# Kernel optimization log

Hardware: AMD Instinct MI355X
Metric: run time of the kernel (lower is better)

## Reference

```python
import jax, jax.numpy as jnp
import numpy as np

DIM = 128
HEADS = 4
DH = 32
SCALE = DH ** -0.5


def _ln(x, g, b):
    m = x.mean(-1, keepdims=True)
    v = x.var(-1, keepdims=True)
    return (x - m) / jnp.sqrt(v + 1e-5) * g + b


def setup_inputs() -> dict:
    key = jax.random.key(0)
    ks = jax.random.split(key, 16)
    B, N, H, W, HK, WK = 2, 6, 48, 48, 24, 24
    d, hd = DIM, HEADS * DH
    p = lambda k, s: (jax.random.normal(k, s, jnp.float32) * 0.02)
    return {
        "q": jax.random.normal(ks[0], (B, N, d, H, W), jnp.float32),
        "k": jax.random.normal(ks[1], (B, N, d, HK, WK), jnp.float32),
        "v": jax.random.normal(ks[2], (B, N, d, HK, WK), jnp.float32),
        "skip": jax.random.normal(ks[3], (B, d, H, W), jnp.float32),
        "lnq_g": jnp.ones(d), "lnq_b": jnp.zeros(d),
        "Wq": p(ks[4], (d, hd)), "bq": jnp.zeros(hd),
        "lnk_g": jnp.ones(d), "lnk_b": jnp.zeros(d),
        "Wk": p(ks[5], (d, hd)), "bk": jnp.zeros(hd),
        "lnv_g": jnp.ones(d), "lnv_b": jnp.zeros(d),
        "Wv": p(ks[6], (d, hd)), "bv": jnp.zeros(hd),
        "Wp": p(ks[7], (hd, d)), "bp": jnp.zeros(d),
        "pre_g": jnp.ones(d), "pre_b": jnp.zeros(d),
        "W1": p(ks[8], (d, 2 * d)), "b1": jnp.zeros(2 * d),
        "W2": p(ks[9], (2 * d, d)), "b2": jnp.zeros(d),
        "post_g": jnp.ones(d), "post_b": jnp.zeros(d),
    }


def reference(q, k, v, skip, lnq_g, lnq_b, Wq, bq, lnk_g, lnk_b, Wk, bk,
              lnv_g, lnv_b, Wv, bv, Wp, bp, pre_g, pre_b, W1, b1, W2, b2,
              post_g, post_b):
    B, N, d, H, W = q.shape
    _, _, _, HK, WK = k.shape
    Q, K = H * W, HK * WK
    # b n d H W -> b n (H W) d
    qx = q.transpose(0, 1, 3, 4, 2).reshape(B, N, Q, d)
    kx = k.transpose(0, 1, 3, 4, 2).reshape(B, N, K, d)
    vx = v.transpose(0, 1, 3, 4, 2).reshape(B, N * K, d)
    # norm + linear projections
    qp = _ln(qx, lnq_g, lnq_b) @ Wq + bq  # (B,N,Q,HEADS*DH)
    kp = _ln(kx, lnk_g, lnk_b) @ Wk + bk
    vp = _ln(vx, lnv_g, lnv_b) @ Wv + bv  # (B,N*K,HEADS*DH)
    # split heads: b ... (m d) -> (b m) ... d
    qp = qp.reshape(B, N, Q, HEADS, DH).transpose(0, 3, 1, 2, 4).reshape(B * HEADS, N, Q, DH)
    kp = kp.reshape(B, N, K, HEADS, DH).transpose(0, 3, 1, 2, 4).reshape(B * HEADS, N, K, DH)
    vp = vp.reshape(B, N * K, HEADS, DH).transpose(0, 2, 1, 3).reshape(B * HEADS, N * K, DH)
    # per-view scores, then softmax jointly over (n K)
    scores = SCALE * jnp.einsum('bnqd,bnkd->bnqk', qp, kp)
    scores = scores.transpose(0, 2, 1, 3).reshape(B * HEADS, Q, N * K)
    a = jax.nn.softmax(scores, axis=-1)
    out = jnp.einsum('bqk,bkd->bqd', a, vp)  # (B*HEADS, Q, DH)
    # merge heads: (b m) Q d -> b Q (m d)
    z = out.reshape(B, HEADS, Q, DH).transpose(0, 2, 1, 3).reshape(B, Q, HEADS * DH)
    z = z @ Wp + bp
    z = z + skip.transpose(0, 2, 3, 1).reshape(B, Q, d)
    z = _ln(z, pre_g, pre_b)
    z = z + (jax.nn.gelu(z @ W1 + b1, approximate=False) @ W2 + b2)
    z = _ln(z, post_g, post_b)
    return z.reshape(B, H, W, d).transpose(0, 3, 1, 2)
```

## Files before the change

### kernel.cpp

```cpp
#include <hip/hip_runtime.h>
#include <cmath>

#define B_    2
#define N_    6
#define D_    128
#define Q_    2304
#define K_    576
#define NK_   3456
#define HEADS_ 4
#define DH_   32
#define SCALE_ 0.17677669529663687f

typedef __attribute__((ext_vector_type(8))) short bf16x8;
typedef __attribute__((ext_vector_type(4))) float f32x4;

static __device__ __forceinline__ unsigned short f2bf(float f) {
  union { float f; unsigned u; } x; x.f = f;
  unsigned u = x.u + 0x7fffu + ((x.u >> 16) & 1u);
  return (unsigned short)(u >> 16);
}
static __device__ __forceinline__ unsigned pkbf(float a, float b) {
  return (unsigned)f2bf(a) | ((unsigned)f2bf(b) << 16);
}

__global__ __launch_bounds__(256) void k_prep_wt(
    const float* __restrict__ Wq, const float* __restrict__ Wk,
    const float* __restrict__ Wv, const float* __restrict__ Wp,
    const float* __restrict__ W1, const float* __restrict__ W2,
    unsigned short* __restrict__ WTq, unsigned short* __restrict__ WTk,
    unsigned short* __restrict__ WTv, unsigned short* __restrict__ WTp,
    unsigned short* __restrict__ WT1, unsigned short* __restrict__ WT2)
{
  __shared__ float tile[32][33];
  const int wb = blockIdx.x, t = threadIdx.x;
  const float* src; unsigned short* dst; int Kd, J, tl;
  if      (wb < 16) { src = Wq; dst = WTq; Kd = 128; J = 128; tl = wb; }
  else if (wb < 32) { src = Wk; dst = WTk; Kd = 128; J = 128; tl = wb - 16; }
  else if (wb < 48) { src = Wv; dst = WTv; Kd = 128; J = 128; tl = wb - 32; }
  else if (wb < 64) { src = Wp; dst = WTp; Kd = 128; J = 128; tl = wb - 48; }
  else if (wb < 96) { src = W1; dst = WT1; Kd = 128; J = 256; tl = wb - 64; }
  else              { src = W2; dst = WT2; Kd = 256; J = 128; tl = wb - 96; }
  const int njt = J >> 5;
  const int tj = tl % njt, tk = tl / njt;
#pragma unroll
  for (int i = 0; i < 4; ++i) {
    int idx = t + 256 * i;
    int r = idx >> 5, c = idx & 31;
    tile[r][c] = src[(size_t)(tk * 32 + r) * J + tj * 32 + c];
  }
  __syncthreads();
#pragma unroll
  for (int i = 0; i < 2; ++i) {
    int idx = t + 256 * i;
    int rr = idx >> 4, c2 = (idx & 15) << 1;
    *(unsigned*)&dst[(size_t)(tj * 32 + rr) * Kd + tk * 32 + c2] =
        pkbf(tile[c2][rr], tile[c2 + 1][rr]);
  }
}

__global__ __launch_bounds__(256) void k_ln_proj_all(
    const float* __restrict__ qin, const float* __restrict__ kin,
    const float* __restrict__ vin,
    const float* __restrict__ lnq_g, const float* __restrict__ lnq_b,
    const float* __restrict__ lnk_g, const float* __restrict__ lnk_b,
    const float* __restrict__ lnv_g, const float* __restrict__ lnv_b,
    const unsigned short* __restrict__ WTq, const unsigned short* __restrict__ WTk,
    const unsigned short* __restrict__ WTv,
    const float* __restrict__ bq, const float* __restrict__ bk,
    const float* __restrict__ bv,
    unsigned short* __restrict__ QPh, unsigned short* __restrict__ KPh,
    unsigned short* __restrict__ VPTh)
{
  __shared__ float xs[32][132];
  __shared__ unsigned short xh[32][136];
  __shared__ float gs[128], bs[128];
  __shared__ float mu[32], rsd[32];
  const int t = threadIdx.x;
  const int bid = blockIdx.x;

  const float* x; const unsigned short* WT; const float* g; const float* bl;
  const float* bias; int S, blk, mode; float osc;
  if (bid < 864)       { mode = 0; blk = bid;        x = qin; WT = WTq; g = lnq_g; bl = lnq_b; bias = bq; S = Q_; osc = SCALE_; }
  else if (bid < 1080) { mode = 0; blk = bid - 864;  x = kin; WT = WTk; g = lnk_g; bl = lnk_b; bias = bk; S = K_; osc = 1.0f; }
  else                 { mode = 1; blk = bid - 1080; x = vin; WT = WTv; g = lnv_g; bl = lnv_b; bias = bv; S = K_; osc = 1.0f; }
  const int ntile = S >> 5;
  const int o  = blk / ntile;
  const int s0 = (blk % ntile) << 5;

  if (t < 128) { gs[t] = g[t]; bs[t] = bl[t]; }
  const float* xb = x + (size_t)o * 128 * (size_t)S + s0;
#pragma unroll
  for (int i = 0; i < 16; ++i) {
    int idx = t + 256 * i;
    int c = idx >> 5, s = idx & 31;
    xs[s][c] = xb[(size_t)c * S + s];
  }
  __syncthreads();
  {
    int s = t >> 3, l8 = t & 7;
    float sum = 0.f, sq = 0.f;
    for (int c = l8; c < 128; c += 8) { float v = xs[s][c]; sum += v; sq += v * v; }
#pragma unroll
    for (int off = 4; off > 0; off >>= 1) {
      sum += __shfl_down(sum, off, 8);
      sq  += __shfl_down(sq,  off, 8);
    }
    if (l8 == 0) {
      float mth = sum * 0.0078125f;
      float var = sq * 0.0078125f - mth * mth;
      mu[s] = mth; rsd[s] = rsqrtf(var + 1e-5f);
    }
  }
  __syncthreads();
#pragma unroll
  for (int i = 0; i < 8; ++i) {
    int idx = t + 256 * i;
    int s = idx >> 6, c2 = (idx & 63) << 1;
    float y0 = (xs[s][c2]     - mu[s]) * rsd[s] * gs[c2]     + bs[c2];
    float y1 = (xs[s][c2 + 1] - mu[s]) * rsd[s] * gs[c2 + 1] + bs[c2 + 1];
    *(unsigned*)&xh[s][c2] = pkbf(y0, y1);
  }
  __syncthreads();
  const int w = t >> 6, lane = t & 63, quad = lane >> 4, l16 = lane & 15;
  const f32x4 zf = {0.f, 0.f, 0.f, 0.f};
  f32x4 acc[2][2] = {{zf, zf}, {zf, zf}};
#pragma unroll
  for (int kc = 0; kc < 4; ++kc) {
    bf16x8 a0 = *(const bf16x8*)&xh[l16][kc * 32 + quad * 8];
    bf16x8 a1 = *(const bf16x8*)&xh[16 + l16][kc * 32 + quad * 8];
    bf16x8 b0 = *(const bf16x8*)&WT[(size_t)(w * 32 + l16) * 128 + kc * 32 + quad * 8];
    bf16x8 b1 = *(const bf16x8*)&WT[(size_t)(w * 32 + 16 + l16) * 128 + kc * 32 + quad * 8];
    acc[0][0] = __builtin_amdgcn_mfma_f32_16x16x32_bf16(a0, b0, acc[0][0], 0, 0, 0);
    acc[0][1] = __builtin_amdgcn_mfma_f32_16x16x32_bf16(a0, b1, acc[0][1], 0, 0, 0);
    acc[1][0] = __builtin_amdgcn_mfma_f32_16x16x32_bf16(a1, b0, acc[1][0], 0, 0, 0);
    acc[1][1] = __builtin_amdgcn_mfma_f32_16x16x32_bf16(a1, b1, acc[1][1], 0, 0, 0);
  }
  if (mode == 0) {
    unsigned short* outh = (bid < 864) ? QPh : KPh;
    __syncthreads();
#pragma unroll
    for (int mt = 0; mt < 2; ++mt)
#pragma unroll
      for (int nt = 0; nt < 2; ++nt) {
        int col = w * 32 + nt * 16 + l16;
        float bc = bias[col];
#pragma unroll
        for (int r = 0; r < 4; ++r)
          xh[mt * 16 + quad * 4 + r][col] = f2bf((acc[mt][nt][r] + bc) * osc);
      }
    __syncthreads();
#pragma unroll
    for (int i = 0; i < 2; ++i) {
      int s = i * 16 + (t >> 4), c8 = (t & 15) << 3;
      *(uint4*)&outh[((size_t)o * S + s0 + s) * 128 + c8] = *(uint4*)&xh[s][c8];
    }
  } else {
    const int b = o / 6, n = o % 6;
#pragma unroll
    for (int mt = 0; mt < 2; ++mt)
#pragma unroll
      for (int nt = 0; nt < 2; ++nt) {
        int col = w * 32 + nt * 16 + l16;
        int hh = col >> 5, dh = col & 31;
        float bc = bias[col];
        ushort4 pk;
        pk.x = f2bf(acc[mt][nt][0] + bc); pk.y = f2bf(acc[mt][nt][1] + bc);
        pk.z = f2bf(acc[mt][nt][2] + bc); pk.w = f2bf(acc[mt][nt][3] + bc);
        int s = n * 576 + s0 + mt * 16 + quad * 4;
        *(ushort4*)&VPTh[((size_t)(b * 4 + hh) * 32 + dh) * (size_t)NK_ + s] = pk;
      }
  }
}

__global__ __launch_bounds__(256) void k_attn_mfma(
    const unsigned short* __restrict__ QPh, const unsigned short* __restrict__ KPh,
    const unsigned short* __restrict__ VPTh, float* __restrict__ PO,
    float* __restrict__ Pl)
{
  __shared__ unsigned short plds[4][2][16][40];
  __shared__ float ol[4][16][32];
  __shared__ float ll[4][2][4][16];
  const int t = threadIdx.x;
  const int w = t >> 6, lane = t & 63;
  const int quad = lane >> 4, l16 = lane & 15;
  const int qt = blockIdx.x % 72;
  const int rest = blockIdx.x / 72;
  const int bhx = rest >> 1, ks = rest & 1;
  const int bb = bhx >> 2, h = bhx & 3;
  const int q0 = qt << 5;

  const unsigned short* vbase = VPTh + (size_t)bhx * 32 * (size_t)NK_;
  const f32x4 zf = {0.f, 0.f, 0.f, 0.f};
  f32x4 o00 = zf, o01 = zf, o10 = zf, o11 = zf;
  float lsum0 = 0.f, lsum1 = 0.f;

  const int m8 = ks * 4 + w;
  int c0 = (108 * m8) >> 3, c1 = (108 * (m8 + 1)) >> 3;

  while (c0 < c1) {
    const int nn = c0 / 18;
    const int cend = min(c1, (nn + 1) * 18);
    const unsigned short* kb = &KPh[((size_t)(bb * 6 + nn) * K_) * 128 + h * 32];
    const unsigned short* qb = &QPh[((size_t)(bb * 6 + nn) * Q_ + q0) * 128 + h * 32];
    bf16x8 qc0 = *(const bf16x8*)&qb[(size_t)l16 * 128 + quad * 8];
    bf16x8 qc1 = *(const bf16x8*)&qb[(size_t)(16 + l16) * 128 + quad * 8];

    int kl = (c0 - nn * 18) << 5;
    bf16x8 kf0 = *(const bf16x8*)&kb[(size_t)(kl + l16) * 128 + quad * 8];
    bf16x8 kf1 = *(const bf16x8*)&kb[(size_t)(kl + 16 + l16) * 128 + quad * 8];
    const unsigned short* vb = vbase + ((size_t)c0 << 5);
    bf16x8 vf0 = *(const bf16x8*)&vb[(size_t)l16 * NK_ + quad * 8];
    bf16x8 vf1 = *(const bf16x8*)&vb[(size_t)(16 + l16) * NK_ + quad * 8];

    for (int kc = c0; kc < cend; ++kc) {
      const int kn = (kc + 1 < cend) ? kc + 1 : kc;
      const int kln = (kn - nn * 18) << 5;
      bf16x8 nk0 = *(const bf16x8*)&kb[(size_t)(kln + l16) * 128 + quad * 8];
      bf16x8 nk1 = *(const bf16x8*)&kb[(size_t)(kln + 16 + l16) * 128 + quad * 8];
      const unsigned short* vbn = vbase + ((size_t)kn << 5);
      bf16x8 nv0 = *(const bf16x8*)&vbn[(size_t)l16 * NK_ + quad * 8];
      bf16x8 nv1 = *(const bf16x8*)&vbn[(size_t)(16 + l16) * NK_ + quad * 8];

      f32x4 s00 = __builtin_amdgcn_mfma_f32_16x16x32_bf16(kf0, qc0, zf, 0, 0, 0);
      f32x4 s01 = __builtin_amdgcn_mfma_f32_16x16x32_bf16(kf1, qc0, zf, 0, 0, 0);
      f32x4 s10 = __builtin_amdgcn_mfma_f32_16x16x32_bf16(kf0, qc1, zf, 0, 0, 0);
      f32x4 s11 = __builtin_amdgcn_mfma_f32_16x16x32_bf16(kf1, qc1, zf, 0, 0, 0);

      float a00 = __expf(fminf(s00.x, 70.f)), a01 = __expf(fminf(s00.y, 70.f));
      float a02 = __expf(fminf(s00.z, 70.f)), a03 = __expf(fminf(s00.w, 70.f));
      float a10 = __expf(fminf(s01.x, 70.f)), a11 = __expf(fminf(s01.y, 70.f));
      float a12 = __expf(fminf(s01.z, 70.f)), a13 = __expf(fminf(s01.w, 70.f));
      lsum0 += (a00 + a01 + a02 + a03) + (a10 + a11 + a12 + a13);
      float b00 = __expf(fminf(s10.x, 70.f)), b01 = __expf(fminf(s10.y, 70.f));
      float b02 = __expf(fminf(s10.z, 70.f)), b03 = __expf(fminf(s10.w, 70.f));
      float b10 = __expf(fminf(s11.x, 70.f)), b11 = __expf(fminf(s11.y, 70.f));
      float b12 = __expf(fminf(s11.z, 70.f)), b13 = __expf(fminf(s11.w, 70.f));
      lsum1 += (b00 + b01 + b02 + b03) + (b10 + b11 + b12 + b13);

      *(unsigned*)&plds[w][0][l16][quad * 4]          = pkbf(a00, a01);
      *(unsigned*)&plds[w][0][l16][quad * 4 + 2]      = pkbf(a02, a03);
      *(unsigned*)&plds[w][0][l16][16 + quad * 4]     = pkbf(a10, a11);
      *(unsigned*)&plds[w][0][l16][16 + quad * 4 + 2] = pkbf(a12, a13);
      *(unsigned*)&plds[w][1][l16][quad * 4]          = pkbf(b00, b01);
      *(unsigned*)&plds[w][1][l16][quad * 4 + 2]      = pkbf(b02, b03);
      *(unsigned*)&plds[w][1][l16][16 + quad * 4]     = pkbf(b10, b11);
      *(unsigned*)&plds[w][1][l16][16 + quad * 4 + 2] = pkbf(b12, b13);
      bf16x8 pf0 = *(const bf16x8*)&plds[w][0][l16][quad * 8];
      bf16x8 pf1 = *(const bf16x8*)&plds[w][1][l16][quad * 8];

      o00 = __builtin_amdgcn_mfma_f32_16x16x32_bf16(pf0, vf0, o00, 0, 0, 0);
      o01 = __builtin_amdgcn_mfma_f32_16x16x32_bf16(pf0, vf1, o01, 0, 0, 0);
      o10 = __builtin_amdgcn_mfma_f32_16x16x32_bf16(pf1, vf0, o10, 0, 0, 0);
      o11 = __builtin_amdgcn_mfma_f32_16x16x32_bf16(pf1, vf1, o11, 0, 0, 0);

      kf0 = nk0; kf1 = nk1; vf0 = nv0; vf1 = nv1;
    }
    c0 = cend;
  }

  ll[w][0][quad][l16] = lsum0;
  ll[w][1][quad][l16] = lsum1;
#pragma unroll
  for (int tt = 0; tt < 2; ++tt) {
    __syncthreads();
    f32x4 t0 = tt ? o10 : o00;
    f32x4 t1 = tt ? o11 : o01;
#pragma unroll
    for (int r = 0; r < 4; ++r) {
      ol[w][quad * 4 + r][l16]      = t0[r];
      ol[w][quad * 4 + r][16 + l16] = t1[r];
    }
    __syncthreads();
    const int q = t >> 4, i16 = t & 15, dd = i16 << 1;
    float a0 = 0.f, a1 = 0.f;
#pragma unroll
    for (int ww = 0; ww < 4; ++ww) { a0 += ol[ww][q][dd]; a1 += ol[ww][q][dd + 1]; }
    float2 r2; r2.x = a0; r2.y = a1;
    *(float2*)&PO[(((size_t)ks * 8 + bhx) * Q_ + q0 + tt * 16 + q) * 32 + dd] = r2;
    if (i16 == 0) {
      float l = 0.f;
#pragma unroll
      for (int ww = 0; ww < 4; ++ww)
#pragma unroll
        for (int qq = 0; qq < 4; ++qq) l += ll[ww][tt][qq][q];
      Pl[((size_t)ks * 8 + bhx) * Q_ + q0 + tt * 16 + q] = l;
    }
  }
}

__global__ __launch_bounds__(256) void k_tail(
    const float* __restrict__ PO, const float* __restrict__ Pl,
    const unsigned short* __restrict__ WTp, const float* __restrict__ bp,
    const float* __restrict__ skip,
    const float* __restrict__ pre_g, const float* __restrict__ pre_b,
    const unsigned short* __restrict__ WT1, const float* __restrict__ b1,
    const unsigned short* __restrict__ WT2, const float* __restrict__ b2,
    const float* __restrict__ post_g, const float* __restrict__ post_b,
    float* __restrict__ out)
{
  __shared__ float xs[32][132];
  __shared__ unsigned short xh[32][136];
  __shared__ unsigned short hb[32][264];
  __shared__ float g1s[128], b1s[128], g2s[128], b2s[128];
  __shared__ float mu[32], rsd[32];
  const int t = threadIdx.x;
  const int row0 = blockIdx.x << 5;
  const int bb = row0 / Q_, hw0 = row0 % Q_;
  const int w = t >> 6, lane = t & 63, quad = lane >> 4, l16 = lane & 15;
  const f32x4 zf = {0.f, 0.f, 0.f, 0.f};

  if (t < 128) { g1s[t] = pre_g[t]; b1s[t] = pre_b[t]; g2s[t] = post_g[t]; b2s[t] = post_b[t]; }
#pragma unroll
  for (int i = 0; i < 8; ++i) {
    int idx = t + 256 * i;
    int s = idx >> 6, c2 = (idx & 63) << 1;
    int q = hw0 + s;
    int h = c2 >> 5, dh = c2 & 31;
    size_t bq = (size_t)(bb * 4 + h) * Q_ + q;
    size_t i0 = bq * 32 + dh;
    float2 p0 = *(const float2*)&PO[i0];
    float2 p1 = *(const float2*)&PO[589824 + i0];
    float inv = 1.f / (Pl[bq] + Pl[18432 + bq]);
    *(unsigned*)&xh[s][c2] = pkbf((p0.x + p1.x) * inv, (p0.y + p1.y) * inv);
  }
  __syncthreads();
  {
    f32x4 acc[2][2] = {{zf, zf}, {zf, zf}};
#pragma unroll
    for (int kc = 0; kc < 4; ++kc) {
      bf16x8 a0 = *(const bf16x8*)&xh[l16][kc * 32 + quad * 8];
      bf16x8 a1 = *(const bf16x8*)&xh[16 + l16][kc * 32 + quad * 8];
      bf16x8 b0 = *(const bf16x8*)&WTp[(size_t)(w * 32 + l16) * 128 + kc * 32 + quad * 8];
      bf16x8 b1v = *(const bf16x8*)&WTp[(size_t)(w * 32 + 16 + l16) * 128 + kc * 32 + quad * 8];
      acc[0][0] = __builtin_amdgcn_mfma_f32_16x16x32_bf16(a0, b0, acc[0][0], 0, 0, 0);
      acc[0][1] = __builtin_amdgcn_mfma_f32_16x16x32_bf16(a0, b1v, acc[0][1], 0, 0, 0);
      acc[1][0] = __builtin_amdgcn_mfma_f32_16x16x32_bf16(a1, b0, acc[1][0], 0, 0, 0);
      acc[1][1] = __builtin_amdgcn_mfma_f32_16x16x32_bf16(a1, b1v, acc[1][1], 0, 0, 0);
    }
#pragma unroll
    for (int mt = 0; mt < 2; ++mt)
#pragma unroll
      for (int nt = 0; nt < 2; ++nt) {
        int col = w * 32 + nt * 16 + l16;
        float bc = bp[col];
        float4 sk = *(const float4*)&skip[((size_t)bb * 128 + col) * Q_ + hw0 + mt * 16 + quad * 4];
        xs[mt * 16 + quad * 4 + 0][col] = acc[mt][nt][0] + bc + sk.x;
        xs[mt * 16 + quad * 4 + 1][col] = acc[mt][nt][1] + bc + sk.y;
        xs[mt * 16 + quad * 4 + 2][col] = acc[mt][nt][2] + bc + sk.z;
        xs[mt * 16 + quad * 4 + 3][col] = acc[mt][nt][3] + bc + sk.w;
      }
  }
  __syncthreads();
  {
    int s = t >> 3, l8 = t & 7;
    float sum = 0.f, sq = 0.f;
    for (int c = l8; c < 128; c += 8) { float v = xs[s][c]; sum += v; sq += v * v; }
#pragma unroll
    for (int off = 4; off > 0; off >>= 1) {
      sum += __shfl_down(sum, off, 8);
      sq  += __shfl_down(sq,  off, 8);
    }
    if (l8 == 0) {
      float mth = sum * 0.0078125f;
      float var = sq * 0.0078125f - mth * mth;
      mu[s] = mth; rsd[s] = rsqrtf(var + 1e-5f);
    }
  }
  __syncthreads();
#pragma unroll
  for (int i = 0; i < 8; ++i) {
    int idx = t + 256 * i;
    int s = idx >> 6, c2 = (idx & 63) << 1;
    float y0 = (xs[s][c2]     - mu[s]) * rsd[s] * g1s[c2]     + b1s[c2];
    float y1 = (xs[s][c2 + 1] - mu[s]) * rsd[s] * g1s[c2 + 1] + b1s[c2 + 1];
    xs[s][c2] = y0; xs[s][c2 + 1] = y1;
    *(unsigned*)&xh[s][c2] = pkbf(y0, y1);
  }
  __syncthreads();
#pragma unroll
  for (int jh = 0; jh < 256; jh += 128) {
    f32x4 acc[2][2] = {{zf, zf}, {zf, zf}};
#pragma unroll
    for (int kc = 0; kc < 4; ++kc) {
      bf16x8 a0 = *(const bf16x8*)&xh[l16][kc * 32 + quad * 8];
      bf16x8 a1 = *(const bf16x8*)&xh[16 + l16][kc * 32 + quad * 8];
      bf16x8 b0 = *(const bf16x8*)&WT1[(size_t)(jh + w * 32 + l16) * 128 + kc * 32 + quad * 8];
      bf16x8 b1v = *(const bf16x8*)&WT1[(size_t)(jh + w * 32 + 16 + l16) * 128 + kc * 32 + quad * 8];
      acc[0][0] = __builtin_amdgcn_mfma_f32_16x16x32_bf16(a0, b0, acc[0][0], 0, 0, 0);
      acc[0][1] = __builtin_amdgcn_mfma_f32_16x16x32_bf16(a0, b1v, acc[0][1], 0, 0, 0);
      acc[1][0] = __builtin_amdgcn_mfma_f32_16x16x32_bf16(a1, b0, acc[1][0], 0, 0, 0);
      acc[1][1] = __builtin_amdgcn_mfma_f32_16x16x32_bf16(a1, b1v, acc[1][1], 0, 0, 0);
    }
#pragma unroll
    for (int mt = 0; mt < 2; ++mt)
#pragma unroll
      for (int nt = 0; nt < 2; ++nt) {
        int col = w * 32 + nt * 16 + l16;
        float bc = b1[jh + col];
#pragma unroll
        for (int r = 0; r < 4; ++r) {
          float hx = acc[mt][nt][r] + bc;
          hb[mt * 16 + quad * 4 + r][jh + col] =
              f2bf(0.5f * hx * (1.f + erff(hx * 0.7071067811865476f)));
        }
      }
  }
  __syncthreads();
  {
    f32x4 acc[2][2] = {{zf, zf}, {zf, zf}};
#pragma unroll
    for (int kc = 0; kc < 8; ++kc) {
      bf16x8 a0 = *(const bf16x8*)&hb[l16][kc * 32 + quad * 8];
      bf16x8 a1 = *(const bf16x8*)&hb[16 + l16][kc * 32 + quad * 8];
      bf16x8 b0 = *(const bf16x8*)&WT2[(size_t)(w * 32 + l16) * 256 + kc * 32 + quad * 8];
      bf16x8 b1v = *(const bf16x8*)&WT2[(size_t)(w * 32 + 16 + l16) * 256 + kc * 32 + quad * 8];
      acc[0][0] = __builtin_amdgcn_mfma_f32_16x16x32_bf16(a0, b0, acc[0][0], 0, 0, 0);
      acc[0][1] = __builtin_amdgcn_mfma_f32_16x16x32_bf16(a0, b1v, acc[0][1], 0, 0, 0);
      acc[1][0] = __builtin_amdgcn_mfma_f32_16x16x32_bf16(a1, b0, acc[1][0], 0, 0, 0);
      acc[1][1] = __builtin_amdgcn_mfma_f32_16x16x32_bf16(a1, b1v, acc[1][1], 0, 0, 0);
    }
#pragma unroll
    for (int mt = 0; mt < 2; ++mt)
#pragma unroll
      for (int nt = 0; nt < 2; ++nt) {
        int col = w * 32 + nt * 16 + l16;
        float bc = b2[col];
#pragma unroll
        for (int r = 0; r < 4; ++r) {
          int row = mt * 16 + quad * 4 + r;
          xs[row][col] = acc[mt][nt][r] + bc + xs[row][col];
        }
      }
  }
  __syncthreads();
  {
    int s = t >> 3, l8 = t & 7;
    float sum = 0.f, sq = 0.f;
    for (int c = l8; c < 128; c += 8) { float v = xs[s][c]; sum += v; sq += v * v; }
#pragma unroll
    for (int off = 4; off > 0; off >>= 1) {
      sum += __shfl_down(sum, off, 8);
      sq  += __shfl_down(sq,  off, 8);
    }
    if (l8 == 0) {
      float mth = sum * 0.0078125f;
      float var = sq * 0.0078125f - mth * mth;
      mu[s] = mth; rsd[s] = rsqrtf(var + 1e-5f);
    }
  }
  __syncthreads();
#pragma unroll
  for (int i = 0; i < 16; ++i) {
    int idx = t + 256 * i;
    int s = idx & 31, c = idx >> 5;
    out[(size_t)bb * (128 * (size_t)Q_) + (size_t)c * Q_ + hw0 + s] =
        (xs[s][c] - mu[s]) * rsd[s] * g2s[c] + b2s[c];
  }
}

extern "C" void kernel_launch(void* const* d_in, const int* in_sizes, int n_in,
                              void* d_out, int out_size, void* d_ws, size_t ws_size,
                              hipStream_t stream) {
  const float* q     = (const float*)d_in[0];
  const float* k     = (const float*)d_in[1];
  const float* v     = (const float*)d_in[2];
  const float* skip  = (const float*)d_in[3];
  const float* lnq_g = (const float*)d_in[4];
  const float* lnq_b = (const float*)d_in[5];
  const float* Wq    = (const float*)d_in[6];
  const float* bq    = (const float*)d_in[7];
  const float* lnk_g = (const float*)d_in[8];
  const float* lnk_b = (const float*)d_in[9];
  const float* Wk    = (const float*)d_in[10];
  const float* bk    = (const float*)d_in[11];
  const float* lnv_g = (const float*)d_in[12];
  const float* lnv_b = (const float*)d_in[13];
  const float* Wv    = (const float*)d_in[14];
  const float* bvv   = (const float*)d_in[15];
  const float* Wp    = (const float*)d_in[16];
  const float* bp    = (const float*)d_in[17];
  const float* pre_g = (const float*)d_in[18];
  const float* pre_b = (const float*)d_in[19];
  const float* W1    = (const float*)d_in[20];
  const float* b1    = (const float*)d_in[21];
  const float* W2    = (const float*)d_in[22];
  const float* b2    = (const float*)d_in[23];
  const float* post_g= (const float*)d_in[24];
  const float* post_b= (const float*)d_in[25];
  float* out = (float*)d_out;

  unsigned short* QPh  = (unsigned short*)d_ws;
  unsigned short* KPh  = QPh + 3538944;
  unsigned short* VPTh = KPh + 884736;
  float* PO  = (float*)(VPTh + 884736);
  float* Pl  = PO + 1179648;
  unsigned short* WTq = (unsigned short*)(Pl + 36864);
  unsigned short* WTk = WTq + 16384;
  unsigned short* WTv = WTk + 16384;
  unsigned short* WTp = WTv + 16384;
  unsigned short* WT1 = WTp + 16384;
  unsigned short* WT2 = WT1 + 32768;

  k_prep_wt<<<dim3(128), dim3(256), 0, stream>>>(Wq, Wk, Wv, Wp, W1, W2,
                                                 WTq, WTk, WTv, WTp, WT1, WT2);
  k_ln_proj_all<<<dim3(1296), dim3(256), 0, stream>>>(
      q, k, v, lnq_g, lnq_b, lnk_g, lnk_b, lnv_g, lnv_b,
      WTq, WTk, WTv, bq, bk, bvv, QPh, KPh, VPTh);
  k_attn_mfma<<<dim3(1152), dim3(256), 0, stream>>>(QPh, KPh, VPTh, PO, Pl);
  k_tail<<<dim3(144), dim3(256), 0, stream>>>(PO, Pl, WTp, bp, skip,
                                              pre_g, pre_b, WT1, b1, WT2, b2,
                                              post_g, post_b, out);
}
```

Before: 176.7 us.

## Split attention keys four ways, widen tail to 512 threads, vectorize loads

The attention kernel now splits the joint key range into 4 partitions instead of 2, doubling the grid to 2304 blocks, and aliases the P staging buffer and the output-reduction buffer in shared memory. The tail kernel runs 512 threads per block, each wave computing 16 columns, and sums four partial outputs and normalizers. The LN-projection load switches to float4 global reads, and the P tile stores become 64-bit LDS writes. More key splits add partial-result traffic and reduction work in exchange for more parallelism on a small problem.

```diff
diff --git a/kernel.cpp b/kernel.cpp
--- a/kernel.cpp
+++ b/kernel.cpp
@@ -90,10 +90,12 @@
   if (t < 128) { gs[t] = g[t]; bs[t] = bl[t]; }
   const float* xb = x + (size_t)o * 128 * (size_t)S + s0;
 #pragma unroll
-  for (int i = 0; i < 16; ++i) {
+  for (int i = 0; i < 4; ++i) {
     int idx = t + 256 * i;
-    int c = idx >> 5, s = idx & 31;
-    xs[s][c] = xb[(size_t)c * S + s];
+    int c = idx >> 3, s4 = (idx & 7) << 2;
+    float4 xv = *(const float4*)&xb[(size_t)c * S + s4];
+    xs[s4 + 0][c] = xv.x; xs[s4 + 1][c] = xv.y;
+    xs[s4 + 2][c] = xv.z; xs[s4 + 3][c] = xv.w;
   }
   __syncthreads();
   {
@@ -177,15 +179,16 @@
     const unsigned short* __restrict__ VPTh, float* __restrict__ PO,
     float* __restrict__ Pl)
 {
-  __shared__ unsigned short plds[4][2][16][40];
-  __shared__ float ol[4][16][32];
+  __shared__ __align__(16) char smem_u[10240];
+  unsigned short (*plds)[2][16][40] = (unsigned short (*)[2][16][40])smem_u;
+  float (*ol)[16][32] = (float (*)[16][32])smem_u;
   __shared__ float ll[4][2][4][16];
   const int t = threadIdx.x;
   const int w = t >> 6, lane = t & 63;
   const int quad = lane >> 4, l16 = lane & 15;
   const int qt = blockIdx.x % 72;
   const int rest = blockIdx.x / 72;
-  const int bhx = rest >> 1, ks = rest & 1;
+  const int bhx = rest >> 2, ks = rest & 3;
   const int bb = bhx >> 2, h = bhx & 3;
   const int q0 = qt << 5;
 
@@ -194,8 +197,8 @@
   f32x4 o00 = zf, o01 = zf, o10 = zf, o11 = zf;
   float lsum0 = 0.f, lsum1 = 0.f;
 
-  const int m8 = ks * 4 + w;
-  int c0 = (108 * m8) >> 3, c1 = (108 * (m8 + 1)) >> 3;
+  const int m16 = ks * 4 + w;
+  int c0 = (108 * m16) >> 4, c1 = (108 * (m16 + 1)) >> 4;
 
   while (c0 < c1) {
     const int nn = c0 / 18;
@@ -237,14 +240,14 @@
       float b12 = __expf(fminf(s11.z, 70.f)), b13 = __expf(fminf(s11.w, 70.f));
       lsum1 += (b00 + b01 + b02 + b03) + (b10 + b11 + b12 + b13);
 
-      *(unsigned*)&plds[w][0][l16][quad * 4]          = pkbf(a00, a01);
-      *(unsigned*)&plds[w][0][l16][quad * 4 + 2]      = pkbf(a02, a03);
-      *(unsigned*)&plds[w][0][l16][16 + quad * 4]     = pkbf(a10, a11);
-      *(unsigned*)&plds[w][0][l16][16 + quad * 4 + 2] = pkbf(a12, a13);
-      *(unsigned*)&plds[w][1][l16][quad * 4]          = pkbf(b00, b01);
-      *(unsigned*)&plds[w][1][l16][quad * 4 + 2]      = pkbf(b02, b03);
-      *(unsigned*)&plds[w][1][l16][16 + quad * 4]     = pkbf(b10, b11);
-      *(unsigned*)&plds[w][1][l16][16 + quad * 4 + 2] = pkbf(b12, b13);
+      uint2 w0a; w0a.x = pkbf(a00, a01); w0a.y = pkbf(a02, a03);
+      uint2 w0b; w0b.x = pkbf(a10, a11); w0b.y = pkbf(a12, a13);
+      uint2 w1a; w1a.x = pkbf(b00, b01); w1a.y = pkbf(b02, b03);
+      uint2 w1b; w1b.x = pkbf(b10, b11); w1b.y = pkbf(b12, b13);
+      *(uint2*)&plds[w][0][l16][quad * 4]      = w0a;
+      *(uint2*)&plds[w][0][l16][16 + quad * 4] = w0b;
+      *(uint2*)&plds[w][1][l16][quad * 4]      = w1a;
+      *(uint2*)&plds[w][1][l16][16 + quad * 4] = w1b;
       bf16x8 pf0 = *(const bf16x8*)&plds[w][0][l16][quad * 8];
       bf16x8 pf1 = *(const bf16x8*)&plds[w][1][l16][quad * 8];
 
@@ -288,7 +291,7 @@
   }
 }
 
-__global__ __launch_bounds__(256) void k_tail(
+__global__ __launch_bounds__(512) void k_tail(
     const float* __restrict__ PO, const float* __restrict__ Pl,
     const unsigned short* __restrict__ WTp, const float* __restrict__ bp,
     const float* __restrict__ skip,
@@ -311,56 +314,56 @@
 
   if (t < 128) { g1s[t] = pre_g[t]; b1s[t] = pre_b[t]; g2s[t] = post_g[t]; b2s[t] = post_b[t]; }
 #pragma unroll
-  for (int i = 0; i < 8; ++i) {
-    int idx = t + 256 * i;
+  for (int i = 0; i < 4; ++i) {
+    int idx = t + 512 * i;
     int s = idx >> 6, c2 = (idx & 63) << 1;
     int q = hw0 + s;
     int h = c2 >> 5, dh = c2 & 31;
     size_t bq = (size_t)(bb * 4 + h) * Q_ + q;
     size_t i0 = bq * 32 + dh;
-    float2 p0 = *(const float2*)&PO[i0];
-    float2 p1 = *(const float2*)&PO[589824 + i0];
-    float inv = 1.f / (Pl[bq] + Pl[18432 + bq]);
-    *(unsigned*)&xh[s][c2] = pkbf((p0.x + p1.x) * inv, (p0.y + p1.y) * inv);
+    float o0 = 0.f, o1 = 0.f, l = 0.f;
+#pragma unroll
+    for (int p = 0; p < 4; ++p) {
+      float2 pp = *(const float2*)&PO[(size_t)p * 589824 + i0];
+      o0 += pp.x; o1 += pp.y;
+      l  += Pl[(size_t)p * 18432 + bq];
+    }
+    float inv = 1.f / l;
+    *(unsigned*)&xh[s][c2] = pkbf(o0 * inv, o1 * inv);
   }
   __syncthreads();
   {
-    f32x4 acc[2][2] = {{zf, zf}, {zf, zf}};
+    f32x4 acc[2] = {zf, zf};
+    const int col = w * 16 + l16;
 #pragma unroll
     for (int kc = 0; kc < 4; ++kc) {
       bf16x8 a0 = *(const bf16x8*)&xh[l16][kc * 32 + quad * 8];
       bf16x8 a1 = *(const bf16x8*)&xh[16 + l16][kc * 32 + quad * 8];
-      bf16x8 b0 = *(const bf16x8*)&WTp[(size_t)(w * 32 + l16) * 128 + kc * 32 + quad * 8];
-      bf16x8 b1v = *(const bf16x8*)&WTp[(size_t)(w * 32 + 16 + l16) * 128 + kc * 32 + quad * 8];
-      acc[0][0] = __builtin_amdgcn_mfma_f32_16x16x32_bf16(a0, b0, acc[0][0], 0, 0, 0);
-      acc[0][1] = __builtin_amdgcn_mfma_f32_16x16x32_bf16(a0, b1v, acc[0][1], 0, 0, 0);
-      acc[1][0] = __builtin_amdgcn_mfma_f32_16x16x32_bf16(a1, b0, acc[1][0], 0, 0, 0);
-      acc[1][1] = __builtin_amdgcn_mfma_f32_16x16x32_bf16(a1, b1v, acc[1][1], 0, 0, 0);
-    }
-#pragma unroll
-    for (int mt = 0; mt < 2; ++mt)
-#pragma unroll
-      for (int nt = 0; nt < 2; ++nt) {
-        int col = w * 32 + nt * 16 + l16;
-        float bc = bp[col];
-        float4 sk = *(const float4*)&skip[((size_t)bb * 128 + col) * Q_ + hw0 + mt * 16 + quad * 4];
-        xs[mt * 16 + quad * 4 + 0][col] = acc[mt][nt][0] + bc + sk.x;
-        xs[mt * 16 + quad * 4 + 1][col] = acc[mt][nt][1] + bc + sk.y;
-        xs[mt * 16 + quad * 4 + 2][col] = acc[mt][nt][2] + bc + sk.z;
-        xs[mt * 16 + quad * 4 + 3][col] = acc[mt][nt][3] + bc + sk.w;
-      }
+      bf16x8 b0 = *(const bf16x8*)&WTp[(size_t)col * 128 + kc * 32 + quad * 8];
+      acc[0] = __builtin_amdgcn_mfma_f32_16x16x32_bf16(a0, b0, acc[0], 0, 0, 0);
+      acc[1] = __builtin_amdgcn_mfma_f32_16x16x32_bf16(a1, b0, acc[1], 0, 0, 0);
+    }
+    float bc = bp[col];
+#pragma unroll
+    for (int mt = 0; mt < 2; ++mt) {
+      float4 sk = *(const float4*)&skip[((size_t)bb * 128 + col) * Q_ + hw0 + mt * 16 + quad * 4];
+      xs[mt * 16 + quad * 4 + 0][col] = acc[mt][0] + bc + sk.x;
+      xs[mt * 16 + quad * 4 + 1][col] = acc[mt][1] + bc + sk.y;
+      xs[mt * 16 + quad * 4 + 2][col] = acc[mt][2] + bc + sk.z;
+      xs[mt * 16 + quad * 4 + 3][col] = acc[mt][3] + bc + sk.w;
+    }
   }
   __syncthreads();
   {
-    int s = t >> 3, l8 = t & 7;
+    int s = t >> 4, lg = t & 15;
     float sum = 0.f, sq = 0.f;
-    for (int c = l8; c < 128; c += 8) { float v = xs[s][c]; sum += v; sq += v * v; }
-#pragma unroll
-    for (int off = 4; off > 0; off >>= 1) {
-      sum += __shfl_down(sum, off, 8);
-      sq  += __shfl_down(sq,  off, 8);
-    }
-    if (l8 == 0) {
+    for (int c = lg; c < 128; c += 16) { float v = xs[s][c]; sum += v; sq += v * v; }
+#pragma unroll
+    for (int off = 8; off > 0; off >>= 1) {
+      sum += __shfl_down(sum, off, 16);
+      sq  += __shfl_down(sq,  off, 16);
+    }
+    if (lg == 0) {
       float mth = sum * 0.0078125f;
       float var = sq * 0.0078125f - mth * mth;
       mu[s] = mth; rsd[s] = rsqrtf(var + 1e-5f);
@@ -368,8 +371,8 @@
   }
   __syncthreads();
 #pragma unroll
-  for (int i = 0; i < 8; ++i) {
-    int idx = t + 256 * i;
+  for (int i = 0; i < 4; ++i) {
+    int idx = t + 512 * i;
     int s = idx >> 6, c2 = (idx & 63) << 1;
     float y0 = (xs[s][c2]     - mu[s]) * rsd[s] * g1s[c2]     + b1s[c2];
     float y1 = (xs[s][c2 + 1] - mu[s]) * rsd[s] * g1s[c2 + 1] + b1s[c2 + 1];
@@ -377,72 +380,62 @@
     *(unsigned*)&xh[s][c2] = pkbf(y0, y1);
   }
   __syncthreads();
-#pragma unroll
-  for (int jh = 0; jh < 256; jh += 128) {
-    f32x4 acc[2][2] = {{zf, zf}, {zf, zf}};
-#pragma unroll
-    for (int kc = 0; kc < 4; ++kc) {
-      bf16x8 a0 = *(const bf16x8*)&xh[l16][kc * 32 + quad * 8];
-      bf16x8 a1 = *(const bf16x8*)&xh[16 + l16][kc * 32 + quad * 8];
-      bf16x8 b0 = *(const bf16x8*)&WT1[(size_t)(jh + w * 32 + l16) * 128 + kc * 32 + quad * 8];
-      bf16x8 b1v = *(const bf16x8*)&WT1[(size_t)(jh + w * 32 + 16 + l16) * 128 + kc * 32 + quad * 8];
-      acc[0][0] = __builtin_amdgcn_mfma_f32_16x16x32_bf16(a0, b0, acc[0][0], 0, 0, 0);
-      acc[0][1] = __builtin_amdgcn_mfma_f32_16x16x32_bf16(a0, b1v, acc[0][1], 0, 0, 0);
-      acc[1][0] = __builtin_amdgcn_mfma_f32_16x16x32_bf16(a1, b0, acc[1][0], 0, 0, 0);
-      acc[1][1] = __builtin_amdgcn_mfma_f32_16x16x32_bf16(a1, b1v, acc[1][1], 0, 0, 0);
-    }
-#pragma unroll
-    for (int mt = 0; mt < 2; ++mt)
-#pragma unroll
-      for (int nt = 0; nt < 2; ++nt) {
-        int col = w * 32 + nt * 16 + l16;
-        float bc = b1[jh + col];
+  {
+#pragma unroll
+    for (int nt = 0; nt < 2; ++nt) {
+      const int col = w * 32 + nt * 16 + l16;
+      f32x4 acc[2] = {zf, zf};
+#pragma unroll
+      for (int kc = 0; kc < 4; ++kc) {
+        bf16x8 a0 = *(const bf16x8*)&xh[l16][kc * 32 + quad * 8];
+        bf16x8 a1 = *(const bf16x8*)&xh[16 + l16][kc * 32 + quad * 8];
+        bf16x8 b0 = *(const bf16x8*)&WT1[(size_t)col * 128 + kc * 32 + quad * 8];
+        acc[0] = __builtin_amdgcn_mfma_f32_16x16x32_bf16(a0, b0, acc[0], 0, 0, 0);
+        acc[1] = __builtin_amdgcn_mfma_f32_16x16x32_bf16(a1, b0, acc[1], 0, 0, 0);
+      }
+      float bc = b1[col];
+#pragma unroll
+      for (int mt = 0; mt < 2; ++mt)
 #pragma unroll
         for (int r = 0; r < 4; ++r) {
-          float hx = acc[mt][nt][r] + bc;
-          hb[mt * 16 + quad * 4 + r][jh + col] =
+          float hx = acc[mt][r] + bc;
+          hb[mt * 16 + quad * 4 + r][col] =
               f2bf(0.5f * hx * (1.f + erff(hx * 0.7071067811865476f)));
         }
-      }
+    }
   }
   __syncthreads();
   {
-    f32x4 acc[2][2] = {{zf, zf}, {zf, zf}};
+    f32x4 acc[2] = {zf, zf};
+    const int col = w * 16 + l16;
 #pragma unroll
     for (int kc = 0; kc < 8; ++kc) {
       bf16x8 a0 = *(const bf16x8*)&hb[l16][kc * 32 + quad * 8];
       bf16x8 a1 = *(const bf16x8*)&hb[16 + l16][kc * 32 + quad * 8];
-      bf16x8 b0 = *(const bf16x8*)&WT2[(size_t)(w * 32 + l16) * 256 + kc * 32 + quad * 8];
-      bf16x8 b1v = *(const bf16x8*)&WT2[(size_t)(w * 32 + 16 + l16) * 256 + kc * 32 + quad * 8];
-      acc[0][0] = __builtin_amdgcn_mfma_f32_16x16x32_bf16(a0, b0, acc[0][0], 0, 0, 0);
-      acc[0][1] = __builtin_amdgcn_mfma_f32_16x16x32_bf16(a0, b1v, acc[0][1], 0, 0, 0);
-      acc[1][0] = __builtin_amdgcn_mfma_f32_16x16x32_bf16(a1, b0, acc[1][0], 0, 0, 0);
-      acc[1][1] = __builtin_amdgcn_mfma_f32_16x16x32_bf16(a1, b1v, acc[1][1], 0, 0, 0);
-    }
+      bf16x8 b0 = *(const bf16x8*)&WT2[(size_t)col * 256 + kc * 32 + quad * 8];
+      acc[0] = __builtin_amdgcn_mfma_f32_16x16x32_bf16(a0, b0, acc[0], 0, 0, 0);
+      acc[1] = __builtin_amdgcn_mfma_f32_16x16x32_bf16(a1, b0, acc[1], 0, 0, 0);
+    }
+    float bc = b2[col];
 #pragma unroll
     for (int mt = 0; mt < 2; ++mt)
 #pragma unroll
-      for (int nt = 0; nt < 2; ++nt) {
-        int col = w * 32 + nt * 16 + l16;
-        float bc = b2[col];
-#pragma unroll
-        for (int r = 0; r < 4; ++r) {
-          int row = mt * 16 + quad * 4 + r;
-          xs[row][col] = acc[mt][nt][r] + bc + xs[row][col];
-        }
+      for (int r = 0; r < 4; ++r) {
+        int row = mt * 16 + quad * 4 + r;
+        xs[row][col] = acc[mt][r] + bc + xs[row][col];
       }
   }
   __syncthreads();
   {
-    int s = t >> 3, l8 = t & 7;
+    int s = t >> 4, lg = t & 15;
     float sum = 0.f, sq = 0.f;
-    for (int c = l8; c < 128; c += 8) { float v = xs[s][c]; sum += v; sq += v * v; }
-#pragma unroll
-    for (int off = 4; off > 0; off >>= 1) {
-      sum += __shfl_down(sum, off, 8);
-      sq  += __shfl_down(sq,  off, 8);
-    }
-    if (l8 == 0) {
+    for (int c = lg; c < 128; c += 16) { float v = xs[s][c]; sum += v; sq += v * v; }
+#pragma unroll
+    for (int off = 8; off > 0; off >>= 1) {
+      sum += __shfl_down(sum, off, 16);
+      sq  += __shfl_down(sq,  off, 16);
+    }
+    if (lg == 0) {
       float mth = sum * 0.0078125f;
       float var = sq * 0.0078125f - mth * mth;
       mu[s] = mth; rsd[s] = rsqrtf(var + 1e-5f);
@@ -450,8 +443,8 @@
   }
   __syncthreads();
 #pragma unroll
-  for (int i = 0; i < 16; ++i) {
-    int idx = t + 256 * i;
+  for (int i = 0; i < 8; ++i) {
+    int idx = t + 512 * i;
     int s = idx & 31, c = idx >> 5;
     out[(size_t)bb * (128 * (size_t)Q_) + (size_t)c * Q_ + hw0 + s] =
         (xs[s][c] - mu[s]) * rsd[s] * g2s[c] + b2s[c];
@@ -493,8 +486,8 @@
   unsigned short* KPh  = QPh + 3538944;
   unsigned short* VPTh = KPh + 884736;
   float* PO  = (float*)(VPTh + 884736);
-  float* Pl  = PO + 1179648;
-  unsigned short* WTq = (unsigned short*)(Pl + 36864);
+  float* Pl  = PO + 2359296;
+  unsigned short* WTq = (unsigned short*)(Pl + 73728);
   unsigned short* WTk = WTq + 16384;
   unsigned short* WTv = WTk + 16384;
   unsigned short* WTp = WTv + 16384;
@@ -506,8 +499,8 @@
   k_ln_proj_all<<<dim3(1296), dim3(256), 0, stream>>>(
       q, k, v, lnq_g, lnq_b, lnk_g, lnk_b, lnv_g, lnv_b,
       WTq, WTk, WTv, bq, bk, bvv, QPh, KPh, VPTh);
-  k_attn_mfma<<<dim3(1152), dim3(256), 0, stream>>>(QPh, KPh, VPTh, PO, Pl);
-  k_tail<<<dim3(144), dim3(256), 0, stream>>>(PO, Pl, WTp, bp, skip,
+  k_attn_mfma<<<dim3(2304), dim3(256), 0, stream>>>(QPh, KPh, VPTh, PO, Pl);
+  k_tail<<<dim3(144), dim3(512), 0, stream>>>(PO, Pl, WTp, bp, skip,
                                               pre_g, pre_b, WT1, b1, WT2, b2,
                                               post_g, post_b, out);
 }
```

Result: no change. 176.5 us (-0.1%).
